# Optimization experiments

Measured on AMD Instinct MI355X. Metric: run time of the kernel, lower is better.

Reference implementation:

```python
import jax, jax.numpy as jnp
import numpy as np

LATENT = 3
HIDDEN = 16
INP = LATENT + 1  # prev_z cat action
B = 1048576


def setup_inputs() -> dict:
    key = jax.random.key(0)
    ks = jax.random.split(key, 11)
    s_ih = 1.0 / np.sqrt(HIDDEN)
    return {
        "prev_z": jax.random.normal(ks[0], (B, LATENT), jnp.float32),
        "action": jax.random.normal(ks[1], (B, 1), jnp.float32),
        "prev_h": jax.random.normal(ks[2], (B, HIDDEN), jnp.float32),
        # GRUCell params (torch layout: [3*H, in] and [3*H, H], gate order r,z,n)
        "W_ih": jax.random.uniform(ks[3], (3 * HIDDEN, INP), jnp.float32, -s_ih, s_ih),
        "W_hh": jax.random.uniform(ks[4], (3 * HIDDEN, HIDDEN), jnp.float32, -s_ih, s_ih),
        "b_ih": jax.random.uniform(ks[5], (3 * HIDDEN,), jnp.float32, -s_ih, s_ih),
        "b_hh": jax.random.uniform(ks[6], (3 * HIDDEN,), jnp.float32, -s_ih, s_ih),
        # prior heads
        "W_mu": jax.random.uniform(ks[7], (LATENT, HIDDEN), jnp.float32, -s_ih, s_ih),
        "b_mu": jax.random.uniform(ks[8], (LATENT,), jnp.float32, -s_ih, s_ih),
        "W_lv": jax.random.uniform(ks[9], (LATENT, HIDDEN), jnp.float32, -s_ih, s_ih),
        "b_lv": jax.random.uniform(ks[10], (LATENT,), jnp.float32, -s_ih, s_ih),
    }


def reference(prev_z, action, prev_h, W_ih, W_hh, b_ih, b_hh, W_mu, b_mu, W_lv, b_lv):
    x = jnp.concatenate([prev_z, action], axis=-1)              # [B, 4]
    gi = x @ W_ih.T + b_ih                                       # [B, 3H]
    gh = prev_h @ W_hh.T + b_hh                                  # [B, 3H]
    i_r, i_z, i_n = jnp.split(gi, 3, axis=-1)
    h_r, h_z, h_n = jnp.split(gh, 3, axis=-1)
    r = jax.nn.sigmoid(i_r + h_r)
    z = jax.nn.sigmoid(i_z + h_z)
    n = jnp.tanh(i_n + r * h_n)
    h = (1.0 - z) * n + z * prev_h                               # [B, H]
    mu = h @ W_mu.T + b_mu                                       # [B, 3]
    logvar = jnp.clip(h @ W_lv.T + b_lv, -5.0, 5.0)              # [B, 3]
    return mu, logvar, h
```

## Files before the change

kernel.cpp:

```cpp
#include <hip/hip_runtime.h>

#define TPB 128
#define WPT 4
#define ROW_H 36
#define LDS_W_HALF (64 * ROW_H)
#define LDS_MU_F32 192
#define LOG2E 1.44269504088896340736f

typedef _Float16 half8 __attribute__((ext_vector_type(8)));
typedef _Float16 half4 __attribute__((ext_vector_type(4)));
typedef __fp16  fp16x2 __attribute__((ext_vector_type(2)));
typedef float f32x4 __attribute__((ext_vector_type(4)));

__device__ __forceinline__ half4 cvt4(float4 v) {
    union { fp16x2 p[2]; half4 h; } u;
    u.p[0] = __builtin_amdgcn_cvt_pkrtz(v.x, v.y);
    u.p[1] = __builtin_amdgcn_cvt_pkrtz(v.z, v.w);
    return u.h;
}
__device__ __forceinline__ half8 cat8(half4 a, half4 b) {
    union { half4 q[2]; half8 o; } u;
    u.q[0] = a; u.q[1] = b;
    return u.o;
}


__global__ __launch_bounds__(64) void prep_kernel(
    const float* __restrict__ W_ih, const float* __restrict__ W_hh,
    const float* __restrict__ b_ih, const float* __restrict__ b_hh,
    const float* __restrict__ W_mu, const float* __restrict__ b_mu,
    const float* __restrict__ W_lv, const float* __restrict__ b_lv,
    void* __restrict__ wsv)
{
    _Float16* wsB = (_Float16*)wsv;
    const int l = threadIdx.x;
    const int col = l & 15, kg = l >> 4;

    #pragma unroll
    for (int t = 0; t < 4; ++t) {
        const int gate = (t == 0) ? col : (t == 1) ? (16 + col) : (32 + col);
        const float scale = (t <= 1) ? -LOG2E : -2.0f * LOG2E;
        #pragma unroll
        for (int i = 0; i < 8; ++i) {
            const int k = kg * 8 + i;
            float v = 0.f;
            if (t <= 1) {
                if (k < 4)       v = W_ih[gate * 4 + k];
                else if (k < 20) v = W_hh[gate * 16 + (k - 4)];
            } else if (t == 2) {
                if (k < 4)       v = W_ih[gate * 4 + k];
            } else {
                if (k >= 4 && k < 20) v = W_hh[gate * 16 + (k - 4)];
            }
            wsB[t * 512 + l * 8 + i] = (_Float16)(v * scale);
        }
    }
    #pragma unroll
    for (int i = 0; i < 8; ++i) {
        const int k = kg * 8 + i;
        wsB[4 * 512 + l * 8 + i] = (_Float16)((k == col + 4) ? 1.f : 0.f);
    }
    #pragma unroll
    for (int i = 0; i < 8; ++i) {
        const int k = kg * 8 + i;
        const int m = col;
        float v = 0.f;
        if (m < 3) {
            if (k < 16)       v = W_mu[m * 16 + k];
            else if (k == 20) v = b_mu[m];
        } else if (m < 6) {
            if (k < 16)       v = W_lv[(m - 3) * 16 + k];
            else if (k == 20) v = b_lv[m - 3];
        }
        wsB[5 * 512 + l * 8 + i] = (_Float16)v;
    }
    if (l < 16) {
        float4* b4 = (float4*)((char*)wsv + 6144);
        b4[l] = make_float4(-LOG2E * (b_ih[l] + b_hh[l]),
                            -LOG2E * (b_ih[16 + l] + b_hh[16 + l]),
                            -2.0f * LOG2E * b_ih[32 + l],
                            -2.0f * LOG2E * b_hh[32 + l]);
    }
}

template<bool EXACT>
__global__ __launch_bounds__(TPB, 6) void rssm_kernel(
    const float* __restrict__ prev_z,
    const float* __restrict__ action,
    const float* __restrict__ prev_h,
    const void*  __restrict__ wsv,
    float* __restrict__ out_mu,
    float* __restrict__ out_lv,
    float* __restrict__ out_h,
    int B)
{
    __shared__ __align__(16) _Float16 Wl[2][LDS_W_HALF];
    __shared__ float MUl[2][LDS_MU_F32];
    __shared__ float LVl[2][LDS_MU_F32];
    const int tid = threadIdx.x;
    const int wid = tid >> 6, lane = tid & 63;
    const int col = lane & 15, kg = lane >> 4;
    const int wbase = (blockIdx.x * 2 + wid) * 64;
    if (!EXACT && wbase >= B) return;

    _Float16* W = Wl[wid];
    float* MU = MUl[wid];
    float* LV = LVl[wid];

    const half8* Bp = (const half8*)wsv;
    const half8 bR  = Bp[lane];
    const half8 bZ  = Bp[64 + lane];
    const half8 bNi = Bp[128 + lane];
    const half8 bNh = Bp[192 + lane];
    const half8 bHp = Bp[256 + lane];
    const half8 a2  = Bp[320 + lane];
    const float4 bias = ((const float4*)((const char*)wsv + 6144))[col];

    {
        half4 z4h; z4h[0] = z4h[1] = z4h[2] = z4h[3] = (_Float16)0.f;
        *(half4*)&W[lane * ROW_H + 20] = z4h;

        const float4* hg = (const float4*)prev_h;
        #pragma unroll
        for (int i = 0; i < 4; ++i) {
            const int fi = i * 64 + lane;
            const int r = fi >> 2, w = fi & 3;
            const int gi = EXACT ? (wbase * 4 + fi) : min(wbase * 4 + fi, B * 4 - 1);
            *(half4*)&W[r * ROW_H + 4 + w * 4] = cvt4(hg[gi]);
        }
        const int zr = EXACT ? (wbase + lane) : min(wbase + lane, B - 1);
        *(half4*)&W[lane * ROW_H] =
            cvt4(make_float4(prev_z[zr * 3 + 0], prev_z[zr * 3 + 1],
                             prev_z[zr * 3 + 2], action[zr]));
    }

    #pragma unroll
    for (int t = 0; t < WPT; ++t) {
        half8 a;
        if (kg < 3) {
            const half4 h0 = *(const half4*)&W[(t * 16 + col) * ROW_H + kg * 8];
            const half4 h1 = *(const half4*)&W[(t * 16 + col) * ROW_H + kg * 8 + 4];
            a = cat8(h0, h1);
        } else {
            half4 zz; zz[0] = zz[1] = zz[2] = zz[3] = (_Float16)0.f;
            a = cat8(zz, zz);
        }

        f32x4 accR  = {bias.x, bias.x, bias.x, bias.x};
        f32x4 accZ  = {bias.y, bias.y, bias.y, bias.y};
        f32x4 accNi = {bias.z, bias.z, bias.z, bias.z};
        f32x4 accNh = {bias.w, bias.w, bias.w, bias.w};
        f32x4 accHp = {0.f, 0.f, 0.f, 0.f};
        accR  = __builtin_amdgcn_mfma_f32_16x16x32_f16(a, bR,  accR,  0, 0, 0);
        accZ  = __builtin_amdgcn_mfma_f32_16x16x32_f16(a, bZ,  accZ,  0, 0, 0);
        accNi = __builtin_amdgcn_mfma_f32_16x16x32_f16(a, bNi, accNi, 0, 0, 0);
        accNh = __builtin_amdgcn_mfma_f32_16x16x32_f16(a, bNh, accNh, 0, 0, 0);
        accHp = __builtin_amdgcn_mfma_f32_16x16x32_f16(a, bHp, accHp, 0, 0, 0);

        #pragma unroll
        for (int q = 0; q < 4; ++q) {
            const float r  = __builtin_amdgcn_rcpf(1.0f + __builtin_amdgcn_exp2f(accR[q]));
            const float z  = __builtin_amdgcn_rcpf(1.0f + __builtin_amdgcn_exp2f(accZ[q]));
            const float ta = fmaf(r, accNh[q], accNi[q]);
            const float n  = fmaf(2.0f,
                                  __builtin_amdgcn_rcpf(1.0f + __builtin_amdgcn_exp2f(ta)),
                                  -1.0f);
            const float hv = fmaf(z, accHp[q] - n, n);
            W[(t * 16 + kg * 4 + q) * ROW_H + 4 + col] = (_Float16)hv;
        }

        half8 b2;
        if (kg < 2) {
            const half4 b0 = *(const half4*)&W[(t * 16 + col) * ROW_H + 4 + kg * 8];
            const half4 b1 = *(const half4*)&W[(t * 16 + col) * ROW_H + 8 + kg * 8];
            b2 = cat8(b0, b1);
        } else {
            half4 zz; zz[0] = zz[1] = zz[2] = zz[3] = (_Float16)0.f;
            b2 = cat8(zz, zz);
            if (kg == 2) b2[4] = (_Float16)1.0f;
        }
        f32x4 acc2 = {0.f, 0.f, 0.f, 0.f};
        acc2 = __builtin_amdgcn_mfma_f32_16x16x32_f16(a2, b2, acc2, 0, 0, 0);

        const int mr = (t * 16 + col) * 3;
        if (kg == 0) {
            MU[mr + 0] = acc2[0];
            MU[mr + 1] = acc2[1];
            MU[mr + 2] = acc2[2];
            LV[mr + 0] = fminf(fmaxf(acc2[3], -5.0f), 5.0f);
        } else if (kg == 1) {
            LV[mr + 1] = fminf(fmaxf(acc2[0], -5.0f), 5.0f);
            LV[mr + 2] = fminf(fmaxf(acc2[1], -5.0f), 5.0f);
        }

        {
            const int r = lane >> 2, w = lane & 3;
            const half4 hh = *(const half4*)&W[(t * 16 + r) * ROW_H + 4 + w * 4];
            const float4 hv4 = make_float4((float)hh[0], (float)hh[1],
                                           (float)hh[2], (float)hh[3]);
            const int orow = wbase + t * 16 + r;
            if (EXACT || orow < B)
                *(float4*)&out_h[(size_t)orow * 16 + w * 4] = hv4;
        }
    }

    if (lane < 48) {
        const int gi = wbase * 3 + lane * 4;
        if (EXACT || gi + 3 < B * 3) {
            *(float4*)&out_mu[gi] = *(const float4*)&MU[lane * 4];
            *(float4*)&out_lv[gi] = *(const float4*)&LV[lane * 4];
        }
    }
}

extern "C" void kernel_launch(void* const* d_in, const int* in_sizes, int n_in,
                              void* d_out, int out_size, void* d_ws, size_t ws_size,
                              hipStream_t stream) {
    const float* prev_z = (const float*)d_in[0];
    const float* action = (const float*)d_in[1];
    const float* prev_h = (const float*)d_in[2];
    const float* W_ih   = (const float*)d_in[3];
    const float* W_hh   = (const float*)d_in[4];
    const float* b_ih   = (const float*)d_in[5];
    const float* b_hh   = (const float*)d_in[6];
    const float* W_mu   = (const float*)d_in[7];
    const float* b_mu   = (const float*)d_in[8];
    const float* W_lv   = (const float*)d_in[9];
    const float* b_lv   = (const float*)d_in[10];

    const int B = in_sizes[0] / 3;
    float* out    = (float*)d_out;
    float* out_mu = out;
    float* out_lv = out + (size_t)3 * B;
    float* out_h  = out + (size_t)6 * B;

    prep_kernel<<<1, 64, 0, stream>>>(W_ih, W_hh, b_ih, b_hh,
                                      W_mu, b_mu, W_lv, b_lv, d_ws);

    const int rows_per_block = 128;
    const int blocks = (B + rows_per_block - 1) / rows_per_block;
    if ((B % rows_per_block) == 0)
        rssm_kernel<true><<<blocks, TPB, 0, stream>>>(prev_z, action, prev_h, d_ws,
                                                      out_mu, out_lv, out_h, B);
    else
        rssm_kernel<false><<<blocks, TPB, 0, stream>>>(prev_z, action, prev_h, d_ws,
                                                       out_mu, out_lv, out_h, B);
}
```

Measured before the change: 42.29 us.

## Load prev_h directly into MFMA A operands with register prefetch, drop LDS staging

Instead of staging prev_h through LDS as fp16, each lane now loads its 8 floats of prev_h straight from global memory into the MFMA A-fragment layout and prefetches the next tile's rows one iteration ahead. The K ordering of the packed weights is changed to put hidden features first and inputs at k=16..19 to match. Only prev_z/action still go through a small LDS buffer. The LDS footprint shrinks and the launch-bounds occupancy hint is removed. The global loads become 32-byte per-lane strided accesses instead of fully coalesced float4 sweeps, and more registers stay live across iterations.

```diff
diff --git a/kernel.cpp b/kernel.cpp
--- a/kernel.cpp
+++ b/kernel.cpp
@@ -2,9 +2,7 @@
 
 #define TPB 128
 #define WPT 4
-#define ROW_H 36
-#define LDS_W_HALF (64 * ROW_H)
-#define LDS_MU_F32 192
+#define HN_STRIDE 20
 #define LOG2E 1.44269504088896340736f
 
 typedef _Float16 half8 __attribute__((ext_vector_type(8)));
@@ -45,12 +43,12 @@
             const int k = kg * 8 + i;
             float v = 0.f;
             if (t <= 1) {
-                if (k < 4)       v = W_ih[gate * 4 + k];
-                else if (k < 20) v = W_hh[gate * 16 + (k - 4)];
+                if (k < 16)                   v = W_hh[gate * 16 + k];
+                else if (k < 20)              v = W_ih[gate * 4 + (k - 16)];
             } else if (t == 2) {
-                if (k < 4)       v = W_ih[gate * 4 + k];
+                if (k >= 16 && k < 20)        v = W_ih[gate * 4 + (k - 16)];
             } else {
-                if (k >= 4 && k < 20) v = W_hh[gate * 16 + (k - 4)];
+                if (k < 16)                   v = W_hh[gate * 16 + k];
             }
             wsB[t * 512 + l * 8 + i] = (_Float16)(v * scale);
         }
@@ -58,7 +56,7 @@
     #pragma unroll
     for (int i = 0; i < 8; ++i) {
         const int k = kg * 8 + i;
-        wsB[4 * 512 + l * 8 + i] = (_Float16)((k == col + 4) ? 1.f : 0.f);
+        wsB[4 * 512 + l * 8 + i] = (_Float16)((k == col) ? 1.f : 0.f);
     }
     #pragma unroll
     for (int i = 0; i < 8; ++i) {
@@ -84,7 +82,7 @@
 }
 
 template<bool EXACT>
-__global__ __launch_bounds__(TPB, 6) void rssm_kernel(
+__global__ __launch_bounds__(TPB) void rssm_kernel(
     const float* __restrict__ prev_z,
     const float* __restrict__ action,
     const float* __restrict__ prev_h,
@@ -94,16 +92,19 @@
     float* __restrict__ out_h,
     int B)
 {
-    __shared__ __align__(16) _Float16 Wl[2][LDS_W_HALF];
-    __shared__ float MUl[2][LDS_MU_F32];
-    __shared__ float LVl[2][LDS_MU_F32];
+    __shared__ __align__(16) _Float16 HNl[2][64 * HN_STRIDE];
+    __shared__ __align__(8)  _Float16 XAl[2][64 * 4];
+    __shared__ float MUl[2][192];
+    __shared__ float LVl[2][192];
+
     const int tid = threadIdx.x;
     const int wid = tid >> 6, lane = tid & 63;
     const int col = lane & 15, kg = lane >> 4;
     const int wbase = (blockIdx.x * 2 + wid) * 64;
     if (!EXACT && wbase >= B) return;
 
-    _Float16* W = Wl[wid];
+    _Float16* HN = HNl[wid];
+    _Float16* XA = XAl[wid];
     float* MU = MUl[wid];
     float* LV = LVl[wid];
 
@@ -117,34 +118,43 @@
     const float4 bias = ((const float4*)((const char*)wsv + 6144))[col];
 
     {
-        half4 z4h; z4h[0] = z4h[1] = z4h[2] = z4h[3] = (_Float16)0.f;
-        *(half4*)&W[lane * ROW_H + 20] = z4h;
-
-        const float4* hg = (const float4*)prev_h;
-        #pragma unroll
-        for (int i = 0; i < 4; ++i) {
-            const int fi = i * 64 + lane;
-            const int r = fi >> 2, w = fi & 3;
-            const int gi = EXACT ? (wbase * 4 + fi) : min(wbase * 4 + fi, B * 4 - 1);
-            *(half4*)&W[r * ROW_H + 4 + w * 4] = cvt4(hg[gi]);
-        }
         const int zr = EXACT ? (wbase + lane) : min(wbase + lane, B - 1);
-        *(half4*)&W[lane * ROW_H] =
+        *(half4*)&XA[lane * 4] =
             cvt4(make_float4(prev_z[zr * 3 + 0], prev_z[zr * 3 + 1],
                              prev_z[zr * 3 + 2], action[zr]));
     }
 
+    half4 zz; zz[0] = zz[1] = zz[2] = zz[3] = (_Float16)0.f;
+
+    float4 p0c, p1c; half4 xac;
+    {
+        const int row = EXACT ? (wbase + col) : min(wbase + col, B - 1);
+        if (kg < 2) {
+            const float4* hp = (const float4*)(prev_h + (size_t)row * 16 + kg * 8);
+            p0c = hp[0]; p1c = hp[1];
+        } else if (kg == 2) {
+            xac = *(const half4*)&XA[col * 4];
+        }
+    }
+
     #pragma unroll
     for (int t = 0; t < WPT; ++t) {
+        float4 p0n, p1n; half4 xan;
+        if (t < WPT - 1) {
+            const int row = EXACT ? (wbase + (t + 1) * 16 + col)
+                                  : min(wbase + (t + 1) * 16 + col, B - 1);
+            if (kg < 2) {
+                const float4* hp = (const float4*)(prev_h + (size_t)row * 16 + kg * 8);
+                p0n = hp[0]; p1n = hp[1];
+            } else if (kg == 2) {
+                xan = *(const half4*)&XA[((t + 1) * 16 + col) * 4];
+            }
+        }
+
         half8 a;
-        if (kg < 3) {
-            const half4 h0 = *(const half4*)&W[(t * 16 + col) * ROW_H + kg * 8];
-            const half4 h1 = *(const half4*)&W[(t * 16 + col) * ROW_H + kg * 8 + 4];
-            a = cat8(h0, h1);
-        } else {
-            half4 zz; zz[0] = zz[1] = zz[2] = zz[3] = (_Float16)0.f;
-            a = cat8(zz, zz);
-        }
+        if (kg < 2)       a = cat8(cvt4(p0c), cvt4(p1c));
+        else if (kg == 2) a = cat8(xac, zz);
+        else              a = cat8(zz, zz);
 
         f32x4 accR  = {bias.x, bias.x, bias.x, bias.x};
         f32x4 accZ  = {bias.y, bias.y, bias.y, bias.y};
@@ -166,16 +176,15 @@
                                   __builtin_amdgcn_rcpf(1.0f + __builtin_amdgcn_exp2f(ta)),
                                   -1.0f);
             const float hv = fmaf(z, accHp[q] - n, n);
-            W[(t * 16 + kg * 4 + q) * ROW_H + 4 + col] = (_Float16)hv;
+            HN[(t * 16 + kg * 4 + q) * HN_STRIDE + col] = (_Float16)hv;
         }
 
         half8 b2;
         if (kg < 2) {
-            const half4 b0 = *(const half4*)&W[(t * 16 + col) * ROW_H + 4 + kg * 8];
-            const half4 b1 = *(const half4*)&W[(t * 16 + col) * ROW_H + 8 + kg * 8];
+            const half4 b0 = *(const half4*)&HN[(t * 16 + col) * HN_STRIDE + kg * 8];
+            const half4 b1 = *(const half4*)&HN[(t * 16 + col) * HN_STRIDE + kg * 8 + 4];
             b2 = cat8(b0, b1);
         } else {
-            half4 zz; zz[0] = zz[1] = zz[2] = zz[3] = (_Float16)0.f;
             b2 = cat8(zz, zz);
             if (kg == 2) b2[4] = (_Float16)1.0f;
         }
@@ -195,13 +204,15 @@
 
         {
             const int r = lane >> 2, w = lane & 3;
-            const half4 hh = *(const half4*)&W[(t * 16 + r) * ROW_H + 4 + w * 4];
+            const half4 hh = *(const half4*)&HN[(t * 16 + r) * HN_STRIDE + w * 4];
             const float4 hv4 = make_float4((float)hh[0], (float)hh[1],
                                            (float)hh[2], (float)hh[3]);
             const int orow = wbase + t * 16 + r;
             if (EXACT || orow < B)
                 *(float4*)&out_h[(size_t)orow * 16 + w * 4] = hv4;
         }
+
+        p0c = p0n; p1c = p1n; xac = xan;
     }
 
     if (lane < 48) {
```

After: 41.89 us. About the same (-0.9%).
